# Kernel optimization log

Measured on AMD Instinct MI355X. Metric: run time of the kernel, lower is better.

## Reference

```python
import jax, jax.numpy as jnp
import numpy as np
from jax import lax

VOCAB = 32000
D_MODEL = 1024
N_LAYERS = 4
D_STATE = 8
D_CONV = 4
EXPAND = 2
D_INNER = EXPAND * D_MODEL          # 2048
DT_RANK = (D_MODEL + 15) // 16      # 64
B, L = 2, 1024


def setup_inputs() -> dict:
    key = jax.random.key(0)
    ks = jax.random.split(key, 20)
    s = 0.02
    inp = {
        "input_ids": jax.random.randint(ks[0], (B, L), 0, VOCAB, dtype=jnp.int32),
        "embed": jax.random.normal(ks[1], (VOCAB, D_MODEL), jnp.float32) * s,
        "in_proj_w": jax.random.normal(ks[2], (N_LAYERS, 2 * D_INNER, D_MODEL), jnp.float32) * s,
        "conv_w": jax.random.normal(ks[3], (N_LAYERS, D_INNER, 1, D_CONV), jnp.float32) * s,
        "conv_b": jnp.zeros((N_LAYERS, D_INNER), jnp.float32),
        "x_proj_w": jax.random.normal(ks[4], (N_LAYERS, DT_RANK + 2 * D_STATE, D_INNER), jnp.float32) * s,
        "dt_proj_w": jax.random.normal(ks[5], (N_LAYERS, D_INNER, DT_RANK), jnp.float32) * s,
        "dt_proj_b": jax.random.normal(ks[6], (N_LAYERS, D_INNER), jnp.float32) * 0.1,
        "A_log": jnp.broadcast_to(jnp.log(jnp.arange(1, D_STATE + 1, dtype=jnp.float32)),
                                  (N_LAYERS, D_INNER, D_STATE)) + 0.0,
        "D": jnp.ones((N_LAYERS, D_INNER), jnp.float32),
        "out_proj_w": jax.random.normal(ks[7], (N_LAYERS, D_MODEL, D_INNER), jnp.float32) * s,
        "ln_g": jnp.ones((N_LAYERS, D_MODEL), jnp.float32),
        "ln_b": jnp.zeros((N_LAYERS, D_MODEL), jnp.float32),
        "fn_g": jnp.ones((D_MODEL,), jnp.float32),
        "fn_b": jnp.zeros((D_MODEL,), jnp.float32),
        "fc_w": jax.random.normal(ks[8], (VOCAB, D_MODEL), jnp.float32) * s,
        "fc_b": jnp.zeros((VOCAB,), jnp.float32),
    }
    return inp


def layer_norm(x, g, b, eps=1e-5):
    mu = jnp.mean(x, -1, keepdims=True)
    var = jnp.var(x, -1, keepdims=True)
    return (x - mu) * lax.rsqrt(var + eps) * g + b


def silu(x):
    return x * jax.nn.sigmoid(x)


def selective_scan(deltaA, deltaBu, C):
    # deltaA, deltaBu: (b,l,d,n); C: (b,l,n) -> y: (b,l,d)
    def step(h, inp):
        dA, dBu, c = inp
        h = dA * h + dBu                       # (b,d,n)
        y = jnp.einsum('bdn,bn->bd', h, c)
        return h, y
    h0 = jnp.zeros(deltaA.shape[:1] + deltaA.shape[2:], deltaA.dtype)
    _, ys = lax.scan(step, h0, (deltaA.transpose(1, 0, 2, 3),
                                deltaBu.transpose(1, 0, 2, 3),
                                C.transpose(1, 0, 2)))
    return ys.transpose(1, 0, 2)


def mamba_block(x, in_proj_w, conv_w, conv_b, x_proj_w, dt_proj_w, dt_proj_b, A_log, D, out_proj_w):
    # x: (b,l,d_model)
    xz = jnp.einsum('bld,ed->ble', x, in_proj_w)          # (b,l,2*di)
    xc, z = jnp.split(xz, 2, axis=-1)
    # causal depthwise conv1d, kernel D_CONV
    xc_ncl = xc.transpose(0, 2, 1)                         # (b,di,l)
    xc_ncl = lax.conv_general_dilated(
        xc_ncl, conv_w, window_strides=(1,), padding=[(D_CONV - 1, 0)],
        feature_group_count=D_INNER, dimension_numbers=('NCH', 'OIH', 'NCH'))
    xc = silu(xc_ncl.transpose(0, 2, 1) + conv_b)          # (b,l,di)
    x_dbl = jnp.einsum('bld,ed->ble', xc, x_proj_w)        # (b,l,dt_rank+2n)
    dt, Bm, Cm = jnp.split(x_dbl, [DT_RANK, DT_RANK + D_STATE], axis=-1)
    dt = jax.nn.softplus(jnp.einsum('blr,dr->bld', dt, dt_proj_w) + dt_proj_b)  # (b,l,di)
    A = -jnp.exp(A_log)                                    # (di,n)
    deltaA = jnp.exp(dt[..., None] * A)                    # (b,l,di,n)
    deltaBu = dt[..., None] * Bm[:, :, None, :] * xc[..., None]
    y = selective_scan(deltaA, deltaBu, Cm)                # (b,l,di)
    y = y + xc * D
    y = y * silu(z)
    return jnp.einsum('ble,de->bld', y, out_proj_w)


def reference(input_ids, embed, in_proj_w, conv_w, conv_b, x_proj_w, dt_proj_w,
              dt_proj_b, A_log, D, out_proj_w, ln_g, ln_b, fn_g, fn_b, fc_w, fc_b):
    x = embed[input_ids]                                   # (b,l,d)
    for i in range(N_LAYERS):
        out = mamba_block(x, in_proj_w[i], conv_w[i], conv_b[i], x_proj_w[i],
                          dt_proj_w[i], dt_proj_b[i], A_log[i], D[i], out_proj_w[i])
        x = layer_norm(out + x, ln_g[i], ln_b[i])
    x = layer_norm(x, fn_g, fn_b)
    logits = jnp.einsum('bld,vd->blv', x, fc_w) + fc_b
    return logits
```

## Files before the change

### kernel.cpp

```cpp
#include <hip/hip_runtime.h>
#include <cstddef>
#include <cstdint>

#define D_MODEL 1024
#define D_INNER 2048
#define DT_RANK 64
#define D_STATE 8
#define NLAYERS 4
#define BATCH 2
#define SEQ 1024
#define M_ROWS (BATCH*SEQ)
#define VOCAB 32000
#define XPAD 128
#define NC 32
#define LC 32
#define XSK 8

typedef __attribute__((ext_vector_type(8))) short short8;
typedef __attribute__((ext_vector_type(4))) float f32x4;

#define GPTR(p) (const __attribute__((address_space(1))) void*)(p)
#define LPTR(p) (__attribute__((address_space(3))) void*)(p)

__device__ __forceinline__ float sigmoidf_(float x) { return 1.f / (1.f + __expf(-x)); }

__device__ __forceinline__ unsigned short f2bf(float f) {
    unsigned u = __float_as_uint(f);
    u += 0x7fffu + ((u >> 16) & 1u);
    return (unsigned short)(u >> 16);
}

__global__ __launch_bounds__(256) void cast_kernel(const float* __restrict__ in,
                                                   unsigned short* __restrict__ out, int n4)
{
    int i = blockIdx.x * 256 + threadIdx.x;
    if (i >= n4) return;
    float4 v = ((const float4*)in)[i];
    ushort4 o;
    o.x = f2bf(v.x); o.y = f2bf(v.y); o.z = f2bf(v.z); o.w = f2bf(v.w);
    ((ushort4*)out)[i] = o;
}

__global__ __launch_bounds__(256) void cast_pad_xproj(const float* __restrict__ in,
                                                      unsigned short* __restrict__ out)
{
    int i = blockIdx.x * 256 + threadIdx.x;
    if (i >= NLAYERS * XPAD * D_INNER / 4) return;
    int col4 = i & (D_INNER / 4 - 1);
    int row = (i >> 9) & (XPAD - 1);
    int layer = i >> 16;
    ushort4 o = {0, 0, 0, 0};
    if (row < 80) {
        float4 v = ((const float4*)(in + ((size_t)layer * 80 + row) * D_INNER))[col4];
        o.x = f2bf(v.x); o.y = f2bf(v.y); o.z = f2bf(v.z); o.w = f2bf(v.w);
    }
    ((ushort4*)out)[i] = o;
}

__global__ __launch_bounds__(256) void gather_kernel(const int* __restrict__ ids,
                                                     const float* __restrict__ embed,
                                                     float* __restrict__ x,
                                                     unsigned short* __restrict__ xb)
{
    int m = blockIdx.x;
    int t = threadIdx.x;
    int id = ids[m];
    float4 v = ((const float4*)(embed + (size_t)id * D_MODEL))[t];
    ((float4*)(x + (size_t)m * D_MODEL))[t] = v;
    ushort4 o;
    o.x = f2bf(v.x); o.y = f2bf(v.y); o.z = f2bf(v.z); o.w = f2bf(v.w);
    ((ushort4*)(xb + (size_t)m * D_MODEL))[t] = o;
}

template<int EPI>
__global__ __launch_bounds__(256) void gemm_bf16_nt(const unsigned short* __restrict__ A, int lda,
                                                    const unsigned short* __restrict__ B, int ldb,
                                                    float* __restrict__ C, int ldc,
                                                    int K, const float* __restrict__ bias)
{
    __shared__ unsigned short As[2][128 * 32];
    __shared__ unsigned short Bs[2][128 * 32];
    const int tid = threadIdx.x;

    const int gm = gridDim.x;
    const int bid = blockIdx.y * gm + blockIdx.x;
    const int q = (gm * gridDim.y) >> 3;
    const int swz = (bid & 7) * q + (bid >> 3);
    const int bm = (swz % gm) * 128, bn = (swz / gm) * 128;

    const int wid = tid >> 6, lane = tid & 63;
    const int wm = (wid >> 1) * 64, wn = (wid & 1) * 64;
    const int lrow = lane & 15, lkg = lane >> 4;

    const int srow = tid >> 2;
    const int ksrc = ((tid & 3) ^ ((srow >> 1) & 3)) * 8;
    const size_t kz = (size_t)blockIdx.z * K;
    const unsigned short* Ag = A + (size_t)(bm + srow) * lda + kz + ksrc;
    const unsigned short* Bg = B + (size_t)(bn + srow) * ldb + kz + ksrc;
    const size_t r64a = (size_t)64 * lda;
    const size_t r64b = (size_t)64 * ldb;

#define STAGE(buf, koff)                                                                              \
    do {                                                                                              \
        __builtin_amdgcn_global_load_lds(GPTR(Ag + (koff)),        LPTR(&As[buf][tid * 8]), 16, 0, 0);\
        __builtin_amdgcn_global_load_lds(GPTR(Ag + r64a + (koff)), LPTR(&As[buf][2048 + tid * 8]), 16, 0, 0);\
        __builtin_amdgcn_global_load_lds(GPTR(Bg + (koff)),        LPTR(&Bs[buf][tid * 8]), 16, 0, 0);\
        __builtin_amdgcn_global_load_lds(GPTR(Bg + r64b + (koff)), LPTR(&Bs[buf][2048 + tid * 8]), 16, 0, 0);\
    } while (0)

    f32x4 acc[4][4];
    #pragma unroll
    for (int i = 0; i < 4; ++i)
        #pragma unroll
        for (int j = 0; j < 4; ++j)
            acc[i][j] = f32x4{0.f, 0.f, 0.f, 0.f};

    STAGE(0, 0);

    int cur = 0;
    for (int k0 = 0; k0 < K; k0 += 32) {
        if (k0 + 32 < K) {
            STAGE(cur ^ 1, k0 + 32);
            asm volatile("s_waitcnt vmcnt(4)" ::: "memory");
        } else {
            asm volatile("s_waitcnt vmcnt(0)" ::: "memory");
        }
        __builtin_amdgcn_s_barrier();
        __builtin_amdgcn_sched_barrier(0);

        short8 af[4], bf[4];
        #pragma unroll
        for (int i = 0; i < 4; ++i) {
            int ra = wm + 16 * i + lrow;
            int pa = lkg ^ ((ra >> 1) & 3);
            af[i] = *(const short8*)(&As[cur][ra * 32 + pa * 8]);
            int rb = wn + 16 * i + lrow;
            int pb = lkg ^ ((rb >> 1) & 3);
            bf[i] = *(const short8*)(&Bs[cur][rb * 32 + pb * 8]);
        }
        #pragma unroll
        for (int i = 0; i < 4; ++i)
            #pragma unroll
            for (int j = 0; j < 4; ++j)
                acc[i][j] = __builtin_amdgcn_mfma_f32_16x16x32_bf16(af[i], bf[j], acc[i][j], 0, 0, 0);

        __builtin_amdgcn_s_barrier();
        cur ^= 1;
    }
#undef STAGE

    if (gridDim.z > 1) C += (size_t)blockIdx.z * M_ROWS * ldc;

    const int crow = bm + wm + lkg * 4;
    const int ccol = bn + wn + lrow;
    #pragma unroll
    for (int i = 0; i < 4; ++i) {
        #pragma unroll
        for (int j = 0; j < 4; ++j) {
            float bv = (EPI == 1 || EPI == 2) ? bias[ccol + 16 * j] : 0.f;
            float* Cp = C + (size_t)(crow + 16 * i) * ldc + ccol + 16 * j;
            #pragma unroll
            for (int r = 0; r < 4; ++r) {
                float v = acc[i][j][r] + bv;
                if (EPI == 1) v = (v > 20.f) ? v : log1pf(__expf(v));
                Cp[(size_t)r * ldc] = v;
            }
        }
    }
}

template<int EPI>
__global__ __launch_bounds__(512) void gemm_bf16_nt256(const unsigned short* __restrict__ A, int lda,
                                                       const unsigned short* __restrict__ B, int ldb,
                                                       float* __restrict__ C, int ldc,
                                                       int K, const float* __restrict__ bias)
{
    __shared__ unsigned short As[2][256 * 32];
    __shared__ unsigned short Bs[2][256 * 32];
    const int tid = threadIdx.x;

    const int gm = gridDim.x;
    const int bid = blockIdx.y * gm + blockIdx.x;
    const int q = (gm * gridDim.y) >> 3;
    const int swz = (bid & 7) * q + (bid >> 3);
    const int bm = (swz % gm) * 256, bn = (swz / gm) * 256;

    const int wid = tid >> 6, lane = tid & 63;
    const int wm = (wid >> 2) * 128, wn = (wid & 3) * 64;
    const int lrow = lane & 15, lkg = lane >> 4;

    const int srow = tid >> 2;
    const int ksrc = ((tid & 3) ^ ((srow >> 1) & 3)) * 8;
    const unsigned short* Ag = A + (size_t)(bm + srow) * lda + ksrc;
    const unsigned short* Bg = B + (size_t)(bn + srow) * ldb + ksrc;
    const size_t r128a = (size_t)128 * lda;
    const size_t r128b = (size_t)128 * ldb;

#define STAGE2(buf, koff)                                                                               \
    do {                                                                                                \
        __builtin_amdgcn_global_load_lds(GPTR(Ag + (koff)),         LPTR(&As[buf][tid * 8]), 16, 0, 0); \
        __builtin_amdgcn_global_load_lds(GPTR(Ag + r128a + (koff)), LPTR(&As[buf][4096 + tid * 8]), 16, 0, 0);\
        __builtin_amdgcn_global_load_lds(GPTR(Bg + (koff)),         LPTR(&Bs[buf][tid * 8]), 16, 0, 0); \
        __builtin_amdgcn_global_load_lds(GPTR(Bg + r128b + (koff)), LPTR(&Bs[buf][4096 + tid * 8]), 16, 0, 0);\
    } while (0)

    f32x4 acc[8][4];
    #pragma unroll
    for (int i = 0; i < 8; ++i)
        #pragma unroll
        for (int j = 0; j < 4; ++j)
            acc[i][j] = f32x4{0.f, 0.f, 0.f, 0.f};

    STAGE2(0, 0);

    int cur = 0;
    for (int k0 = 0; k0 < K; k0 += 32) {
        if (k0 + 32 < K) {
            STAGE2(cur ^ 1, k0 + 32);
            asm volatile("s_waitcnt vmcnt(4)" ::: "memory");
        } else {
            asm volatile("s_waitcnt vmcnt(0)" ::: "memory");
        }
        __builtin_amdgcn_s_barrier();
        __builtin_amdgcn_sched_barrier(0);

        short8 af[8], bf[4];
        #pragma unroll
        for (int j = 0; j < 4; ++j) {
            int rb = wn + 16 * j + lrow;
            int pb = lkg ^ ((rb >> 1) & 3);
            bf[j] = *(const short8*)(&Bs[cur][rb * 32 + pb * 8]);
        }
        #pragma unroll
        for (int i = 0; i < 8; ++i) {
            int ra = wm + 16 * i + lrow;
            int pa = lkg ^ ((ra >> 1) & 3);
            af[i] = *(const short8*)(&As[cur][ra * 32 + pa * 8]);
        }
        #pragma unroll
        for (int i = 0; i < 8; ++i)
            #pragma unroll
            for (int j = 0; j < 4; ++j)
                acc[i][j] = __builtin_amdgcn_mfma_f32_16x16x32_bf16(af[i], bf[j], acc[i][j], 0, 0, 0);

        __builtin_amdgcn_s_barrier();
        cur ^= 1;
    }
#undef STAGE2

    const int crow = bm + wm + lkg * 4;
    const int ccol = bn + wn + lrow;
    #pragma unroll
    for (int i = 0; i < 8; ++i) {
        #pragma unroll
        for (int j = 0; j < 4; ++j) {
            float bv = (EPI == 2) ? bias[ccol + 16 * j] : 0.f;
            float* Cp = C + (size_t)(crow + 16 * i) * ldc + ccol + 16 * j;
            #pragma unroll
            for (int r = 0; r < 4; ++r)
                Cp[(size_t)r * ldc] = acc[i][j][r] + bv;
        }
    }
}

__global__ __launch_bounds__(256) void reduce_xdbl(const float* __restrict__ part,
                                                   float* __restrict__ xdbl,
                                                   unsigned short* __restrict__ xdbl_b)
{
    int i = blockIdx.x * 256 + threadIdx.x;
    float4 s = ((const float4*)part)[i];
    #pragma unroll
    for (int z = 1; z < XSK; ++z) {
        float4 v = ((const float4*)part)[(size_t)z * (M_ROWS * XPAD / 4) + i];
        s.x += v.x; s.y += v.y; s.z += v.z; s.w += v.w;
    }
    ((float4*)xdbl)[i] = s;
    ushort4 o;
    o.x = f2bf(s.x); o.y = f2bf(s.y); o.z = f2bf(s.z); o.w = f2bf(s.w);
    ((ushort4*)xdbl_b)[i] = o;
}

__global__ __launch_bounds__(256) void conv_silu_kernel(const float* __restrict__ xz,
                                                        const float* __restrict__ cw,
                                                        const float* __restrict__ cb,
                                                        float* __restrict__ xc,
                                                        unsigned short* __restrict__ xcb)
{
    int idx = blockIdx.x * 256 + threadIdx.x;
    int d = idx & (D_INNER - 1);
    int m = idx >> 11;
    int l = m & (SEQ - 1);
    int b = m >> 10;
    float w0 = cw[d * 4 + 0], w1 = cw[d * 4 + 1], w2 = cw[d * 4 + 2], w3 = cw[d * 4 + 3];
    float s = cb[d];
    const float* base = xz + ((size_t)b * SEQ) * (2 * D_INNER) + d;
    if (l - 3 >= 0) s += base[(size_t)(l - 3) * (2 * D_INNER)] * w0;
    if (l - 2 >= 0) s += base[(size_t)(l - 2) * (2 * D_INNER)] * w1;
    if (l - 1 >= 0) s += base[(size_t)(l - 1) * (2 * D_INNER)] * w2;
    s += base[(size_t)l * (2 * D_INNER)] * w3;
    float v = s * sigmoidf_(s);
    xc[(size_t)m * D_INNER + d] = v;
    xcb[(size_t)m * D_INNER + d] = f2bf(v);
}

__global__ __launch_bounds__(256) void scan_partial(const float* __restrict__ dt,
                                                    const float* __restrict__ xdbl,
                                                    const float* __restrict__ xc,
                                                    const float* __restrict__ A_log,
                                                    float* __restrict__ H,
                                                    float* __restrict__ P)
{
    const int tid = threadIdx.x;
    const int b = blockIdx.x & 1;
    const int c = (blockIdx.x >> 1) & (NC - 1);
    const int d = ((blockIdx.x >> 6) << 8) + tid;

    __shared__ float Bs[LC][8];
    {
        int r = tid >> 3, n = tid & 7;
        Bs[r][n] = xdbl[(size_t)(b * SEQ + c * LC + r) * XPAD + DT_RANK + n];
    }
    __syncthreads();

    float An[8];
    #pragma unroll
    for (int n = 0; n < 8; ++n) An[n] = -__expf(A_log[d * 8 + n]);
    float h[8] = {0.f,0.f,0.f,0.f,0.f,0.f,0.f,0.f};
    float p[8] = {1.f,1.f,1.f,1.f,1.f,1.f,1.f,1.f};

    const float* dtp = dt + (size_t)(b * SEQ + c * LC) * D_INNER + d;
    const float* xcp = xc + (size_t)(b * SEQ + c * LC) * D_INNER + d;
    for (int l = 0; l < LC; ++l) {
        float dtv = dtp[(size_t)l * D_INNER];
        float ux  = dtv * xcp[(size_t)l * D_INNER];
        #pragma unroll
        for (int n = 0; n < 8; ++n) {
            float dA = __expf(dtv * An[n]);
            h[n] = dA * h[n] + Bs[l][n] * ux;
            p[n] *= dA;
        }
    }
    size_t base = (size_t)((b * NC + c) * 8) * D_INNER + d;
    #pragma unroll
    for (int n = 0; n < 8; ++n) {
        H[base + (size_t)n * D_INNER] = h[n];
        P[base + (size_t)n * D_INNER] = p[n];
    }
}

__global__ __launch_bounds__(256) void scan_combine(const float* __restrict__ H,
                                                    float* __restrict__ P )
{
    int idx = blockIdx.x * 256 + threadIdx.x;
    int d = idx & (D_INNER - 1);
    int n = (idx >> 11) & 7;
    int b = idx >> 14;
    float hp = 0.f;
    for (int c = 0; c < NC; ++c) {
        size_t base = (size_t)((b * NC + c) * 8 + n) * D_INNER + d;
        float Pv = P[base], Hv = H[base];
        P[base] = hp;
        hp = Pv * hp + Hv;
    }
}

__global__ __launch_bounds__(256) void scan_final(const float* __restrict__ dt,
                                                  const float* __restrict__ xdbl,
                                                  const float* __restrict__ xc,
                                                  const float* __restrict__ xz,
                                                  const float* __restrict__ A_log,
                                                  const float* __restrict__ Dp,
                                                  const float* __restrict__ h0,
                                                  unsigned short* __restrict__ yb)
{
    const int tid = threadIdx.x;
    const int b = blockIdx.x & 1;
    const int c = (blockIdx.x >> 1) & (NC - 1);
    const int d = ((blockIdx.x >> 6) << 8) + tid;

    __shared__ float Bs[LC][8];
    __shared__ float Cs[LC][8];
    {
        int r = tid >> 3, n = tid & 7;
        size_t xrow = (size_t)(b * SEQ + c * LC + r) * XPAD;
        Bs[r][n] = xdbl[xrow + DT_RANK + n];
        Cs[r][n] = xdbl[xrow + DT_RANK + 8 + n];
    }
    __syncthreads();

    float An[8], h[8];
    size_t base = (size_t)((b * NC + c) * 8) * D_INNER + d;
    #pragma unroll
    for (int n = 0; n < 8; ++n) {
        An[n] = -__expf(A_log[d * 8 + n]);
        h[n] = h0[base + (size_t)n * D_INNER];
    }
    const float Dv = Dp[d];

    const float* dtp = dt + (size_t)(b * SEQ + c * LC) * D_INNER + d;
    const float* xcp = xc + (size_t)(b * SEQ + c * LC) * D_INNER + d;
    const float* zp  = xz + (size_t)(b * SEQ + c * LC) * (2 * D_INNER) + D_INNER + d;
    unsigned short* ybp = yb + (size_t)(b * SEQ + c * LC) * D_INNER + d;

    for (int l = 0; l < LC; ++l) {
        float dtv = dtp[(size_t)l * D_INNER];
        float xcv = xcp[(size_t)l * D_INNER];
        float zv  = zp[(size_t)l * (2 * D_INNER)];
        float ux = dtv * xcv;
        float acc = 0.f;
        #pragma unroll
        for (int n = 0; n < 8; ++n) {
            float dA = __expf(dtv * An[n]);
            h[n] = dA * h[n] + Bs[l][n] * ux;
            acc += h[n] * Cs[l][n];
        }
        float yv = (acc + xcv * Dv) * (zv * sigmoidf_(zv));
        ybp[(size_t)l * D_INNER] = f2bf(yv);
    }
}

template<bool ADD>
__global__ __launch_bounds__(256) void ln_kernel(const float* __restrict__ extra,
                                                 const float* __restrict__ xin,
                                                 float* __restrict__ xout,
                                                 unsigned short* __restrict__ xbout,
                                                 const float* __restrict__ g,
                                                 const float* __restrict__ bb)
{
    int m = blockIdx.x;
    int t = threadIdx.x;
    float4 v = ((const float4*)(xin + (size_t)m * D_MODEL))[t];
    if (ADD) {
        float4 e = ((const float4*)(extra + (size_t)m * D_MODEL))[t];
        v.x += e.x; v.y += e.y; v.z += e.z; v.w += e.w;
    }
    float s  = v.x + v.y + v.z + v.w;
    float s2 = v.x * v.x + v.y * v.y + v.z * v.z + v.w * v.w;
    for (int off = 32; off; off >>= 1) {
        s  += __shfl_down(s, off);
        s2 += __shfl_down(s2, off);
    }
    __shared__ float red[8];
    int wid = t >> 6, lane = t & 63;
    if (lane == 0) { red[wid] = s; red[wid + 4] = s2; }
    __syncthreads();
    if (t == 0) {
        float a  = red[0] + red[1] + red[2] + red[3];
        float b2 = red[4] + red[5] + red[6] + red[7];
        float mu = a * (1.f / D_MODEL);
        red[0] = mu;
        red[4] = b2 * (1.f / D_MODEL) - mu * mu;
    }
    __syncthreads();
    float mu = red[0];
    float rs = rsqrtf(red[4] + 1e-5f);
    float4 gg = ((const float4*)g)[t];
    float4 bv = ((const float4*)bb)[t];
    float4 o;
    o.x = (v.x - mu) * rs * gg.x + bv.x;
    o.y = (v.y - mu) * rs * gg.y + bv.y;
    o.z = (v.z - mu) * rs * gg.z + bv.z;
    o.w = (v.w - mu) * rs * gg.w + bv.w;
    ((float4*)(xout + (size_t)m * D_MODEL))[t] = o;
    ushort4 ob;
    ob.x = f2bf(o.x); ob.y = f2bf(o.y); ob.z = f2bf(o.z); ob.w = f2bf(o.w);
    ((ushort4*)(xbout + (size_t)m * D_MODEL))[t] = ob;
}

extern "C" void kernel_launch(void* const* d_in, const int* in_sizes, int n_in,
                              void* d_out, int out_size, void* d_ws, size_t ws_size,
                              hipStream_t stream)
{
    const int*   ids      = (const int*)d_in[0];
    const float* embed    = (const float*)d_in[1];
    const float* in_proj  = (const float*)d_in[2];
    const float* conv_w   = (const float*)d_in[3];
    const float* conv_b   = (const float*)d_in[4];
    const float* x_proj   = (const float*)d_in[5];
    const float* dt_w     = (const float*)d_in[6];
    const float* dt_b     = (const float*)d_in[7];
    const float* A_log    = (const float*)d_in[8];
    const float* Dp       = (const float*)d_in[9];
    const float* out_proj = (const float*)d_in[10];
    const float* ln_g     = (const float*)d_in[11];
    const float* ln_b     = (const float*)d_in[12];
    const float* fn_g     = (const float*)d_in[13];
    const float* fn_b     = (const float*)d_in[14];
    const float* fc_w     = (const float*)d_in[15];
    const float* fc_b     = (const float*)d_in[16];
    float* logits = (float*)d_out;

    float* ws = (float*)d_ws;
    float* x     = ws;
    float* xz    = x + (size_t)M_ROWS * D_MODEL;
    float* xc    = xz + (size_t)M_ROWS * 2 * D_INNER;
    float* xdbl  = xc + (size_t)M_ROWS * D_INNER;
    float* dtbuf = xdbl + (size_t)M_ROWS * XPAD;
    float* tmp   = dtbuf + (size_t)M_ROWS * D_INNER;
    float* xpart = tmp + (size_t)M_ROWS * D_MODEL;

    float* Hbuf = tmp;
    float* Pbuf = tmp + (size_t)BATCH * NC * D_STATE * D_INNER;

    unsigned short* xb     = (unsigned short*)(xpart + (size_t)XSK * M_ROWS * XPAD);
    unsigned short* yb     = xb + (size_t)M_ROWS * D_MODEL;
    unsigned short* xcb    = yb + (size_t)M_ROWS * D_INNER;
    unsigned short* xdbl_b = xcb + (size_t)M_ROWS * D_INNER;
    unsigned short* wb_in  = xdbl_b + (size_t)M_ROWS * XPAD;
    unsigned short* wb_out = wb_in + (size_t)NLAYERS * 2 * D_INNER * D_MODEL;
    unsigned short* wb_fc  = wb_out + (size_t)NLAYERS * D_MODEL * D_INNER;
    unsigned short* wb_x   = wb_fc + (size_t)VOCAB * D_MODEL;
    unsigned short* wb_dt  = wb_x + (size_t)NLAYERS * XPAD * D_INNER;

    {
        int n4 = NLAYERS * 2 * D_INNER * D_MODEL / 4;
        cast_kernel<<<(n4 + 255) / 256, 256, 0, stream>>>(in_proj, wb_in, n4);
        n4 = NLAYERS * D_MODEL * D_INNER / 4;
        cast_kernel<<<(n4 + 255) / 256, 256, 0, stream>>>(out_proj, wb_out, n4);
        n4 = VOCAB * D_MODEL / 4;
        cast_kernel<<<(n4 + 255) / 256, 256, 0, stream>>>(fc_w, wb_fc, n4);
        n4 = NLAYERS * D_INNER * DT_RANK / 4;
        cast_kernel<<<(n4 + 255) / 256, 256, 0, stream>>>(dt_w, wb_dt, n4);
        n4 = NLAYERS * XPAD * D_INNER / 4;
        cast_pad_xproj<<<(n4 + 255) / 256, 256, 0, stream>>>(x_proj, wb_x);
    }

    gather_kernel<<<M_ROWS, 256, 0, stream>>>(ids, embed, x, xb);

    for (int i = 0; i < NLAYERS; ++i) {
        const unsigned short* W_in_b  = wb_in + (size_t)i * 2 * D_INNER * D_MODEL;
        const unsigned short* W_out_b = wb_out + (size_t)i * D_MODEL * D_INNER;
        const unsigned short* W_x_b   = wb_x + (size_t)i * XPAD * D_INNER;
        const unsigned short* W_dt_b  = wb_dt + (size_t)i * D_INNER * DT_RANK;
        const float* cw    = conv_w + (size_t)i * D_INNER * 4;
        const float* cb    = conv_b + (size_t)i * D_INNER;
        const float* b_dt  = dt_b + (size_t)i * D_INNER;
        const float* Al    = A_log + (size_t)i * D_INNER * D_STATE;
        const float* Dl    = Dp + (size_t)i * D_INNER;
        const float* g     = ln_g + (size_t)i * D_MODEL;
        const float* bb    = ln_b + (size_t)i * D_MODEL;

        gemm_bf16_nt<0><<<dim3(M_ROWS / 128, 2 * D_INNER / 128), 256, 0, stream>>>(
            xb, D_MODEL, W_in_b, D_MODEL, xz, 2 * D_INNER, D_MODEL, nullptr);

        conv_silu_kernel<<<(M_ROWS * D_INNER) / 256, 256, 0, stream>>>(xz, cw, cb, xc, xcb);

        gemm_bf16_nt<0><<<dim3(M_ROWS / 128, 1, XSK), 256, 0, stream>>>(
            xcb, D_INNER, W_x_b, D_INNER, xpart, XPAD, D_INNER / XSK, nullptr);
        reduce_xdbl<<<(M_ROWS * XPAD / 4) / 256, 256, 0, stream>>>(xpart, xdbl, xdbl_b);

        gemm_bf16_nt<1><<<dim3(M_ROWS / 128, D_INNER / 128), 256, 0, stream>>>(
            xdbl_b, XPAD, W_dt_b, DT_RANK, dtbuf, D_INNER, DT_RANK, b_dt);

        scan_partial<<<BATCH * NC * (D_INNER / 256), 256, 0, stream>>>(
            dtbuf, xdbl, xc, Al, Hbuf, Pbuf);
        scan_combine<<<(BATCH * D_STATE * D_INNER) / 256, 256, 0, stream>>>(Hbuf, Pbuf);
        scan_final<<<BATCH * NC * (D_INNER / 256), 256, 0, stream>>>(
            dtbuf, xdbl, xc, xz, Al, Dl, Pbuf, yb);

        gemm_bf16_nt<0><<<dim3(M_ROWS / 128, D_MODEL / 128), 256, 0, stream>>>(
            yb, D_INNER, W_out_b, D_INNER, tmp, D_MODEL, D_INNER, nullptr);

        ln_kernel<true><<<M_ROWS, 256, 0, stream>>>(tmp, x, x, xb, g, bb);
    }

    ln_kernel<false><<<M_ROWS, 256, 0, stream>>>(nullptr, x, tmp, xb, fn_g, fn_b);

    gemm_bf16_nt256<2><<<dim3(M_ROWS / 256, VOCAB / 256), 512, 0, stream>>>(
        xb, D_MODEL, wb_fc, D_MODEL, logits, VOCAB, D_MODEL, fc_b);
}
```

Baseline: 1.001 ms.

## Store xz, xc and dt intermediates in bf16 and raise MFMA wave priority

The in_proj GEMM now writes xz as bf16, and the dt_proj GEMM writes softplus(dt) as bf16. The conv kernel drops its fp32 xc output, so the scan kernels read bf16 dt, xc and z instead of fp32. This roughly halves the memory traffic of these elementwise and scan stages, at the cost of bf16 rounding error in the intermediates. The GEMM inner loops also wrap their MFMA blocks in s_setprio(1)/s_setprio(0) to favour the math phase when waves are scheduled.

New measurement: 1.010 ms. Within noise of the previous version (+0.8%).

```diff
diff --git a/kernel.cpp b/kernel.cpp
--- a/kernel.cpp
+++ b/kernel.cpp
@@ -29,6 +29,9 @@
     u += 0x7fffu + ((u >> 16) & 1u);
     return (unsigned short)(u >> 16);
 }
+__device__ __forceinline__ float bf2f(unsigned short u) {
+    return __uint_as_float((unsigned)u << 16);
+}
 
 __global__ __launch_bounds__(256) void cast_kernel(const float* __restrict__ in,
                                                    unsigned short* __restrict__ out, int n4)
@@ -75,7 +78,7 @@
 template<int EPI>
 __global__ __launch_bounds__(256) void gemm_bf16_nt(const unsigned short* __restrict__ A, int lda,
                                                     const unsigned short* __restrict__ B, int ldb,
-                                                    float* __restrict__ C, int ldc,
+                                                    void* __restrict__ Cv, int ldc,
                                                     int K, const float* __restrict__ bias)
 {
     __shared__ unsigned short As[2][128 * 32];
@@ -138,38 +141,43 @@
             int pb = lkg ^ ((rb >> 1) & 3);
             bf[i] = *(const short8*)(&Bs[cur][rb * 32 + pb * 8]);
         }
+        __builtin_amdgcn_s_setprio(1);
         #pragma unroll
         for (int i = 0; i < 4; ++i)
             #pragma unroll
             for (int j = 0; j < 4; ++j)
                 acc[i][j] = __builtin_amdgcn_mfma_f32_16x16x32_bf16(af[i], bf[j], acc[i][j], 0, 0, 0);
+        __builtin_amdgcn_s_setprio(0);
 
         __builtin_amdgcn_s_barrier();
         cur ^= 1;
     }
 #undef STAGE
 
-    if (gridDim.z > 1) C += (size_t)blockIdx.z * M_ROWS * ldc;
-
     const int crow = bm + wm + lkg * 4;
     const int ccol = bn + wn + lrow;
     #pragma unroll
     for (int i = 0; i < 4; ++i) {
         #pragma unroll
         for (int j = 0; j < 4; ++j) {
-            float bv = (EPI == 1 || EPI == 2) ? bias[ccol + 16 * j] : 0.f;
-            float* Cp = C + (size_t)(crow + 16 * i) * ldc + ccol + 16 * j;
+            float bv = (EPI == 2 || EPI == 3) ? bias[ccol + 16 * j] : 0.f;
             #pragma unroll
             for (int r = 0; r < 4; ++r) {
                 float v = acc[i][j][r] + bv;
-                if (EPI == 1) v = (v > 20.f) ? v : log1pf(__expf(v));
-                Cp[(size_t)r * ldc] = v;
+                size_t off = (size_t)(crow + 16 * i + r) * ldc + ccol + 16 * j;
+                if (EPI == 0) {
+                    ((float*)Cv)[(size_t)blockIdx.z * M_ROWS * ldc + off] = v;
+                } else if (EPI == 2) {
+                    ((float*)Cv)[off] = v;
+                } else {
+                    if (EPI == 3) v = (v > 20.f) ? v : log1pf(__expf(v));
+                    ((unsigned short*)Cv)[off] = f2bf(v);
+                }
             }
         }
     }
 }
 
-template<int EPI>
 __global__ __launch_bounds__(512) void gemm_bf16_nt256(const unsigned short* __restrict__ A, int lda,
                                                        const unsigned short* __restrict__ B, int ldb,
                                                        float* __restrict__ C, int ldc,
@@ -237,11 +245,13 @@
             int pa = lkg ^ ((ra >> 1) & 3);
             af[i] = *(const short8*)(&As[cur][ra * 32 + pa * 8]);
         }
+        __builtin_amdgcn_s_setprio(1);
         #pragma unroll
         for (int i = 0; i < 8; ++i)
             #pragma unroll
             for (int j = 0; j < 4; ++j)
                 acc[i][j] = __builtin_amdgcn_mfma_f32_16x16x32_bf16(af[i], bf[j], acc[i][j], 0, 0, 0);
+        __builtin_amdgcn_s_setprio(0);
 
         __builtin_amdgcn_s_barrier();
         cur ^= 1;
@@ -254,7 +264,7 @@
     for (int i = 0; i < 8; ++i) {
         #pragma unroll
         for (int j = 0; j < 4; ++j) {
-            float bv = (EPI == 2) ? bias[ccol + 16 * j] : 0.f;
+            float bv = bias[ccol + 16 * j];
             float* Cp = C + (size_t)(crow + 16 * i) * ldc + ccol + 16 * j;
             #pragma unroll
             for (int r = 0; r < 4; ++r)
@@ -280,10 +290,9 @@
     ((ushort4*)xdbl_b)[i] = o;
 }
 
-__global__ __launch_bounds__(256) void conv_silu_kernel(const float* __restrict__ xz,
+__global__ __launch_bounds__(256) void conv_silu_kernel(const unsigned short* __restrict__ xzb,
                                                         const float* __restrict__ cw,
                                                         const float* __restrict__ cb,
-                                                        float* __restrict__ xc,
                                                         unsigned short* __restrict__ xcb)
 {
     int idx = blockIdx.x * 256 + threadIdx.x;
@@ -293,19 +302,18 @@
     int b = m >> 10;
     float w0 = cw[d * 4 + 0], w1 = cw[d * 4 + 1], w2 = cw[d * 4 + 2], w3 = cw[d * 4 + 3];
     float s = cb[d];
-    const float* base = xz + ((size_t)b * SEQ) * (2 * D_INNER) + d;
-    if (l - 3 >= 0) s += base[(size_t)(l - 3) * (2 * D_INNER)] * w0;
-    if (l - 2 >= 0) s += base[(size_t)(l - 2) * (2 * D_INNER)] * w1;
-    if (l - 1 >= 0) s += base[(size_t)(l - 1) * (2 * D_INNER)] * w2;
-    s += base[(size_t)l * (2 * D_INNER)] * w3;
+    const unsigned short* base = xzb + ((size_t)b * SEQ) * (2 * D_INNER) + d;
+    if (l - 3 >= 0) s += bf2f(base[(size_t)(l - 3) * (2 * D_INNER)]) * w0;
+    if (l - 2 >= 0) s += bf2f(base[(size_t)(l - 2) * (2 * D_INNER)]) * w1;
+    if (l - 1 >= 0) s += bf2f(base[(size_t)(l - 1) * (2 * D_INNER)]) * w2;
+    s += bf2f(base[(size_t)l * (2 * D_INNER)]) * w3;
     float v = s * sigmoidf_(s);
-    xc[(size_t)m * D_INNER + d] = v;
     xcb[(size_t)m * D_INNER + d] = f2bf(v);
 }
 
-__global__ __launch_bounds__(256) void scan_partial(const float* __restrict__ dt,
+__global__ __launch_bounds__(256) void scan_partial(const unsigned short* __restrict__ dtb,
                                                     const float* __restrict__ xdbl,
-                                                    const float* __restrict__ xc,
+                                                    const unsigned short* __restrict__ xcb,
                                                     const float* __restrict__ A_log,
                                                     float* __restrict__ H,
                                                     float* __restrict__ P)
@@ -315,10 +323,10 @@
     const int c = (blockIdx.x >> 1) & (NC - 1);
     const int d = ((blockIdx.x >> 6) << 8) + tid;
 
-    __shared__ float Bs[LC][8];
+    __shared__ float Bsm[LC][8];
     {
         int r = tid >> 3, n = tid & 7;
-        Bs[r][n] = xdbl[(size_t)(b * SEQ + c * LC + r) * XPAD + DT_RANK + n];
+        Bsm[r][n] = xdbl[(size_t)(b * SEQ + c * LC + r) * XPAD + DT_RANK + n];
     }
     __syncthreads();
 
@@ -328,15 +336,15 @@
     float h[8] = {0.f,0.f,0.f,0.f,0.f,0.f,0.f,0.f};
     float p[8] = {1.f,1.f,1.f,1.f,1.f,1.f,1.f,1.f};
 
-    const float* dtp = dt + (size_t)(b * SEQ + c * LC) * D_INNER + d;
-    const float* xcp = xc + (size_t)(b * SEQ + c * LC) * D_INNER + d;
+    const unsigned short* dtp = dtb + (size_t)(b * SEQ + c * LC) * D_INNER + d;
+    const unsigned short* xcp = xcb + (size_t)(b * SEQ + c * LC) * D_INNER + d;
     for (int l = 0; l < LC; ++l) {
-        float dtv = dtp[(size_t)l * D_INNER];
-        float ux  = dtv * xcp[(size_t)l * D_INNER];
+        float dtv = bf2f(dtp[(size_t)l * D_INNER]);
+        float ux  = dtv * bf2f(xcp[(size_t)l * D_INNER]);
         #pragma unroll
         for (int n = 0; n < 8; ++n) {
             float dA = __expf(dtv * An[n]);
-            h[n] = dA * h[n] + Bs[l][n] * ux;
+            h[n] = dA * h[n] + Bsm[l][n] * ux;
             p[n] *= dA;
         }
     }
@@ -364,10 +372,10 @@
     }
 }
 
-__global__ __launch_bounds__(256) void scan_final(const float* __restrict__ dt,
+__global__ __launch_bounds__(256) void scan_final(const unsigned short* __restrict__ dtb,
                                                   const float* __restrict__ xdbl,
-                                                  const float* __restrict__ xc,
-                                                  const float* __restrict__ xz,
+                                                  const unsigned short* __restrict__ xcb,
+                                                  const unsigned short* __restrict__ xzb,
                                                   const float* __restrict__ A_log,
                                                   const float* __restrict__ Dp,
                                                   const float* __restrict__ h0,
@@ -378,13 +386,13 @@
     const int c = (blockIdx.x >> 1) & (NC - 1);
     const int d = ((blockIdx.x >> 6) << 8) + tid;
 
-    __shared__ float Bs[LC][8];
-    __shared__ float Cs[LC][8];
+    __shared__ float Bsm[LC][8];
+    __shared__ float Csm[LC][8];
     {
         int r = tid >> 3, n = tid & 7;
         size_t xrow = (size_t)(b * SEQ + c * LC + r) * XPAD;
-        Bs[r][n] = xdbl[xrow + DT_RANK + n];
-        Cs[r][n] = xdbl[xrow + DT_RANK + 8 + n];
+        Bsm[r][n] = xdbl[xrow + DT_RANK + n];
+        Csm[r][n] = xdbl[xrow + DT_RANK + 8 + n];
     }
     __syncthreads();
 
@@ -397,22 +405,22 @@
     }
     const float Dv = Dp[d];
 
-    const float* dtp = dt + (size_t)(b * SEQ + c * LC) * D_INNER + d;
-    const float* xcp = xc + (size_t)(b * SEQ + c * LC) * D_INNER + d;
-    const float* zp  = xz + (size_t)(b * SEQ + c * LC) * (2 * D_INNER) + D_INNER + d;
+    const unsigned short* dtp = dtb + (size_t)(b * SEQ + c * LC) * D_INNER + d;
+    const unsigned short* xcp = xcb + (size_t)(b * SEQ + c * LC) * D_INNER + d;
+    const unsigned short* zp  = xzb + (size_t)(b * SEQ + c * LC) * (2 * D_INNER) + D_INNER + d;
     unsigned short* ybp = yb + (size_t)(b * SEQ + c * LC) * D_INNER + d;
 
     for (int l = 0; l < LC; ++l) {
-        float dtv = dtp[(size_t)l * D_INNER];
-        float xcv = xcp[(size_t)l * D_INNER];
-        float zv  = zp[(size_t)l * (2 * D_INNER)];
+        float dtv = bf2f(dtp[(size_t)l * D_INNER]);
+        float xcv = bf2f(xcp[(size_t)l * D_INNER]);
+        float zv  = bf2f(zp[(size_t)l * (2 * D_INNER)]);
         float ux = dtv * xcv;
         float acc = 0.f;
         #pragma unroll
         for (int n = 0; n < 8; ++n) {
             float dA = __expf(dtv * An[n]);
-            h[n] = dA * h[n] + Bs[l][n] * ux;
-            acc += h[n] * Cs[l][n];
+            h[n] = dA * h[n] + Bsm[l][n] * ux;
+            acc += h[n] * Csm[l][n];
         }
         float yv = (acc + xcv * Dv) * (zv * sigmoidf_(zv));
         ybp[(size_t)l * D_INNER] = f2bf(yv);
@@ -492,11 +500,8 @@
 
     float* ws = (float*)d_ws;
     float* x     = ws;
-    float* xz    = x + (size_t)M_ROWS * D_MODEL;
-    float* xc    = xz + (size_t)M_ROWS * 2 * D_INNER;
-    float* xdbl  = xc + (size_t)M_ROWS * D_INNER;
-    float* dtbuf = xdbl + (size_t)M_ROWS * XPAD;
-    float* tmp   = dtbuf + (size_t)M_ROWS * D_INNER;
+    float* xdbl  = x + (size_t)M_ROWS * D_MODEL;
+    float* tmp   = xdbl + (size_t)M_ROWS * XPAD;
     float* xpart = tmp + (size_t)M_ROWS * D_MODEL;
 
     float* Hbuf = tmp;
@@ -504,8 +509,10 @@
 
     unsigned short* xb     = (unsigned short*)(xpart + (size_t)XSK * M_ROWS * XPAD);
     unsigned short* yb     = xb + (size_t)M_ROWS * D_MODEL;
-    unsigned short* xcb    = yb + (size_t)M_ROWS * D_INNER;
-    unsigned short* xdbl_b = xcb + (size_t)M_ROWS * D_INNER;
+    unsigned short* xzb    = yb + (size_t)M_ROWS * D_INNER;
+    unsigned short* xcb    = xzb + (size_t)M_ROWS * 2 * D_INNER;
+    unsigned short* dtb    = xcb + (size_t)M_ROWS * D_INNER;
+    unsigned short* xdbl_b = dtb + (size_t)M_ROWS * D_INNER;
     unsigned short* wb_in  = xdbl_b + (size_t)M_ROWS * XPAD;
     unsigned short* wb_out = wb_in + (size_t)NLAYERS * 2 * D_INNER * D_MODEL;
     unsigned short* wb_fc  = wb_out + (size_t)NLAYERS * D_MODEL * D_INNER;
@@ -540,23 +547,23 @@
         const float* g     = ln_g + (size_t)i * D_MODEL;
         const float* bb    = ln_b + (size_t)i * D_MODEL;
 
-        gemm_bf16_nt<0><<<dim3(M_ROWS / 128, 2 * D_INNER / 128), 256, 0, stream>>>(
-            xb, D_MODEL, W_in_b, D_MODEL, xz, 2 * D_INNER, D_MODEL, nullptr);
-
-        conv_silu_kernel<<<(M_ROWS * D_INNER) / 256, 256, 0, stream>>>(xz, cw, cb, xc, xcb);
+        gemm_bf16_nt<1><<<dim3(M_ROWS / 128, 2 * D_INNER / 128), 256, 0, stream>>>(
+            xb, D_MODEL, W_in_b, D_MODEL, xzb, 2 * D_INNER, D_MODEL, nullptr);
+
+        conv_silu_kernel<<<(M_ROWS * D_INNER) / 256, 256, 0, stream>>>(xzb, cw, cb, xcb);
 
         gemm_bf16_nt<0><<<dim3(M_ROWS / 128, 1, XSK), 256, 0, stream>>>(
             xcb, D_INNER, W_x_b, D_INNER, xpart, XPAD, D_INNER / XSK, nullptr);
         reduce_xdbl<<<(M_ROWS * XPAD / 4) / 256, 256, 0, stream>>>(xpart, xdbl, xdbl_b);
 
-        gemm_bf16_nt<1><<<dim3(M_ROWS / 128, D_INNER / 128), 256, 0, stream>>>(
-            xdbl_b, XPAD, W_dt_b, DT_RANK, dtbuf, D_INNER, DT_RANK, b_dt);
+        gemm_bf16_nt<3><<<dim3(M_ROWS / 128, D_INNER / 128), 256, 0, stream>>>(
+            xdbl_b, XPAD, W_dt_b, DT_RANK, dtb, D_INNER, DT_RANK, b_dt);
 
         scan_partial<<<BATCH * NC * (D_INNER / 256), 256, 0, stream>>>(
-            dtbuf, xdbl, xc, Al, Hbuf, Pbuf);
+            dtb, xdbl, xcb, Al, Hbuf, Pbuf);
         scan_combine<<<(BATCH * D_STATE * D_INNER) / 256, 256, 0, stream>>>(Hbuf, Pbuf);
         scan_final<<<BATCH * NC * (D_INNER / 256), 256, 0, stream>>>(
-            dtbuf, xdbl, xc, xz, Al, Dl, Pbuf, yb);
+            dtb, xdbl, xcb, xzb, Al, Dl, Pbuf, yb);
 
         gemm_bf16_nt<0><<<dim3(M_ROWS / 128, D_MODEL / 128), 256, 0, stream>>>(
             yb, D_INNER, W_out_b, D_INNER, tmp, D_MODEL, D_INNER, nullptr);
@@ -566,6 +573,6 @@
 
     ln_kernel<false><<<M_ROWS, 256, 0, stream>>>(nullptr, x, tmp, xb, fn_g, fn_b);
 
-    gemm_bf16_nt256<2><<<dim3(M_ROWS / 256, VOCAB / 256), 512, 0, stream>>>(
+    gemm_bf16_nt256<<<dim3(M_ROWS / 256, VOCAB / 256), 512, 0, stream>>>(
         xb, D_MODEL, wb_fc, D_MODEL, logits, VOCAB, D_MODEL, fc_b);
 }
```
